# Optimization experiments

Measured on AMD Instinct MI355X. Metric: run time of the kernel, lower is better.

Reference implementation:

```python
import jax, jax.numpy as jnp
import numpy as np

N_NODES = 50000
N_EDGES = 800000
D_IN = 96
D_HID = 96
D_OUT = 96


def _mean_agg(x, src, dst, n_nodes):
    # mean over in-neighbors: agg[v] = mean_{(u->v) in E} x[u]
    msg = x[src]  # [E, d] irregular gather
    summed = jax.ops.segment_sum(msg, dst, num_segments=n_nodes)  # [N, d]
    deg = jax.ops.segment_sum(jnp.ones((src.shape[0],), x.dtype), dst,
                              num_segments=n_nodes)  # [N]
    return summed / jnp.maximum(deg, 1.0)[:, None]


def _sage_conv(x, src, dst, W_self, W_neigh, b):
    agg = _mean_agg(x, src, dst, x.shape[0])
    return x @ W_self + agg @ W_neigh + b


def setup_inputs() -> dict:
    key = jax.random.key(0)
    ks = jax.random.split(key, 9)
    s = 0.05
    return {
        "x": jax.random.normal(ks[0], (N_NODES, D_IN), jnp.float32),
        "src": jax.random.randint(ks[1], (N_EDGES,), 0, N_NODES),
        "dst": jax.random.randint(ks[2], (N_EDGES,), 0, N_NODES),
        "W_self1": jax.random.normal(ks[3], (D_IN, D_HID), jnp.float32) * s,
        "W_neigh1": jax.random.normal(ks[4], (D_IN, D_HID), jnp.float32) * s,
        "b1": jnp.zeros((D_HID,), jnp.float32),
        "W_self2": jax.random.normal(ks[5], (D_HID, D_OUT), jnp.float32) * s,
        "W_neigh2": jax.random.normal(ks[6], (D_HID, D_OUT), jnp.float32) * s,
        "b2": jnp.zeros((D_OUT,), jnp.float32),
    }


def reference(x, src, dst, W_self1, W_neigh1, b1, W_self2, W_neigh2, b2):
    h = _sage_conv(x, src, dst, W_self1, W_neigh1, b1)
    h = jax.nn.relu(h)
    h = _sage_conv(h, src, dst, W_self2, W_neigh2, b2)
    return h
```

## Files before the change

### kernel.cpp

```cpp
#include <hip/hip_runtime.h>
#include <cstdint>
#include <cstddef>

#define NN 50000
#define NE 800000
#define D 96

#define NBUCK 512
#define BSH 7
#define NBU ((NN + 127) >> 7)
#define TILE 8192
#define NTILE ((NE + TILE - 1) / TILE)
#define MAXB 5120

#define AGB 32
#define AGW 1024

typedef __attribute__((ext_vector_type(8))) short bf16x8;
typedef __attribute__((ext_vector_type(4))) float f32x4;


__global__ void bucket_hist(const int* __restrict__ dst, int* __restrict__ bucketCnt) {
    __shared__ int h[NBUCK];
    for (int i = threadIdx.x; i < NBUCK; i += 256) h[i] = 0;
    __syncthreads();
    const int stride = gridDim.x * 256 * 4;
    for (int i = (blockIdx.x * 256 + (int)threadIdx.x) * 4; i < NE; i += stride) {
        int4 d4 = *(const int4*)(dst + i);
        atomicAdd(&h[d4.x >> BSH], 1);
        atomicAdd(&h[d4.y >> BSH], 1);
        atomicAdd(&h[d4.z >> BSH], 1);
        atomicAdd(&h[d4.w >> BSH], 1);
    }
    __syncthreads();
    for (int i = threadIdx.x; i < NBUCK; i += 256)
        if (h[i]) atomicAdd(&bucketCnt[i], h[i]);
}

__global__ void bucket_scan(const int* __restrict__ bucketCnt, int* __restrict__ bucketBase,
                            int* __restrict__ bucketCur) {
    __shared__ int sm[NBUCK];
    const int t = threadIdx.x;
    const int v = bucketCnt[t];
    sm[t] = v;
    __syncthreads();
    for (int s = 1; s < NBUCK; s <<= 1) {
        int u = (t >= s) ? sm[t - s] : 0;
        __syncthreads();
        sm[t] += u;
        __syncthreads();
    }
    const int excl = sm[t] - v;
    bucketBase[t] = excl;
    bucketCur[t] = excl;
}

__launch_bounds__(512)
__global__ void bin_edges(const int* __restrict__ dst, const int* __restrict__ src,
                          int* __restrict__ bucketCur, uint2* __restrict__ pairBuf) {
    __shared__ int hist[NBUCK];
    __shared__ int segStart[NBUCK];
    __shared__ int lcur[NBUCK];
    __shared__ int segBase[NBUCK];
    __shared__ uint2 lpair[TILE];
    const int t = threadIdx.x;
    const int e0 = blockIdx.x * TILE;
    const int cnt = (NE - e0 < TILE) ? (NE - e0) : TILE;

    for (int i = t; i < NBUCK; i += 512) hist[i] = 0;
    __syncthreads();

    for (int i = t * 4; i < cnt; i += 512 * 4) {
        if (i + 3 < cnt) {
            int4 d4 = *(const int4*)(dst + e0 + i);
            atomicAdd(&hist[d4.x >> BSH], 1);
            atomicAdd(&hist[d4.y >> BSH], 1);
            atomicAdd(&hist[d4.z >> BSH], 1);
            atomicAdd(&hist[d4.w >> BSH], 1);
        } else {
            for (int k = i; k < cnt; ++k) atomicAdd(&hist[dst[e0 + k] >> BSH], 1);
        }
    }
    __syncthreads();

    {
        const int v = hist[t];
        segStart[t] = v;
        __syncthreads();
        for (int s = 1; s < NBUCK; s <<= 1) {
            int u = (t >= s) ? segStart[t - s] : 0;
            __syncthreads();
            segStart[t] += u;
            __syncthreads();
        }
        int excl = segStart[t] - v;
        __syncthreads();
        segStart[t] = excl;
        lcur[t] = excl;
    }
    __syncthreads();

    for (int i = t * 4; i < cnt; i += 512 * 4) {
        if (i + 3 < cnt) {
            int4 d4 = *(const int4*)(dst + e0 + i);
            int4 s4 = *(const int4*)(src + e0 + i);
            int p0 = atomicAdd(&lcur[d4.x >> BSH], 1); lpair[p0] = make_uint2(d4.x, s4.x);
            int p1 = atomicAdd(&lcur[d4.y >> BSH], 1); lpair[p1] = make_uint2(d4.y, s4.y);
            int p2 = atomicAdd(&lcur[d4.z >> BSH], 1); lpair[p2] = make_uint2(d4.z, s4.z);
            int p3 = atomicAdd(&lcur[d4.w >> BSH], 1); lpair[p3] = make_uint2(d4.w, s4.w);
        } else {
            for (int k = i; k < cnt; ++k) {
                int d = dst[e0 + k], s = src[e0 + k];
                int p = atomicAdd(&lcur[d >> BSH], 1);
                lpair[p] = make_uint2(d, s);
            }
        }
    }
    __syncthreads();

    {
        int c = hist[t];
        segBase[t] = c ? atomicAdd(&bucketCur[t], c) : 0;
    }
    __syncthreads();

    for (int k = t; k < cnt; k += 512) {
        uint2 p = lpair[k];
        int b = (int)p.x >> BSH;
        pairBuf[(size_t)segBase[b] + (k - segStart[b])] = p;
    }
}

__global__ void csr_build(const uint2* __restrict__ pairBuf, const int* __restrict__ bucketBase,
                          const int* __restrict__ bucketCnt, int* __restrict__ startv,
                          int* __restrict__ csr) {
    __shared__ int h[128], ls[128], cur[128];
    __shared__ int lsrc[MAXB];
    const int b = blockIdx.x;
    const int t = threadIdx.x;
    const int lo = bucketBase[b];
    int cnt = bucketCnt[b];
    if (cnt > MAXB) cnt = MAXB;
    const int node0 = b << BSH;

    if (t < 128) h[t] = 0;
    __syncthreads();
    for (int k = t; k < cnt; k += 256)
        atomicAdd(&h[(int)pairBuf[lo + k].x - node0], 1);
    __syncthreads();
    if (t < 128) ls[t] = h[t];
    __syncthreads();
    for (int s = 1; s < 128; s <<= 1) {
        int u = (t >= s && t < 128) ? ls[t - s] : 0;
        __syncthreads();
        if (t < 128) ls[t] += u;
        __syncthreads();
    }
    if (t < 128) {
        int excl = ls[t] - h[t];
        cur[t] = excl;
        int node = node0 + t;
        if (node < NN) startv[node] = lo + excl;
    }
    __syncthreads();
    for (int k = t; k < cnt; k += 256) {
        uint2 p = pairBuf[lo + k];
        int pos = atomicAdd(&cur[(int)p.x - node0], 1);
        lsrc[pos] = (int)p.y;
    }
    __syncthreads();
    for (int k = t; k < cnt; k += 256) csr[lo + k] = lsrc[k];
}


__device__ inline uint32_t pack2_bf16(float a, float b) {
    uint32_t ua = __float_as_uint(a), ub = __float_as_uint(b);
    ua = (ua + 0x7fffu + ((ua >> 16) & 1u)) >> 16;
    ub = (ub + 0x7fffu + ((ub >> 16) & 1u)) >> 16;
    return ua | (ub << 16);
}

__device__ inline unsigned short pack1_bf16(float a) {
    uint32_t ua = __float_as_uint(a);
    return (unsigned short)((ua + 0x7fffu + ((ua >> 16) & 1u)) >> 16);
}

__device__ inline float bf_lo(uint32_t w) { return __uint_as_float(w << 16); }
__device__ inline float bf_hi(uint32_t w) { return __uint_as_float(w & 0xffff0000u); }


__global__ void repack_both(const float* __restrict__ Ws1, const float* __restrict__ Wn1,
                            const float* __restrict__ Ws2, const float* __restrict__ Wn2,
                            uint32_t* __restrict__ bfg1, uint32_t* __restrict__ bfg2) {
    int t = blockIdx.x * 256 + threadIdx.x;
    if (t >= 4608) return;
    const int layer = (t >= 2304);
    int tt = t - layer * 2304;
    const int isWn = (tt >= 1152);
    const float* __restrict__ W = layer ? (isWn ? Wn2 : Ws2) : (isWn ? Wn1 : Ws1);
    uint32_t* __restrict__ Bfg = layer ? bfg2 : bfg1;
    tt = isWn ? tt - 1152 : tt;
    int s = tt / 384;
    int r = tt - s * 384;
    int nt6 = r >> 6;
    int l = r & 63;
    int col = nt6 * 16 + (l & 15);
    int k0 = 32 * s + 8 * (l >> 4);
    float v[8];
#pragma unroll
    for (int j = 0; j < 8; ++j) v[j] = W[(k0 + j) * D + col];
    uint4 o;
    o.x = pack2_bf16(v[0], v[1]);
    o.y = pack2_bf16(v[2], v[3]);
    o.z = pack2_bf16(v[4], v[5]);
    o.w = pack2_bf16(v[6], v[7]);
    int nt = nt6 + (isWn ? 6 : 0);
    int slot = (s * 12 + nt) * 64 + l;
    *(uint4*)(Bfg + (size_t)slot * 4) = o;
}


__launch_bounds__(256, 2)
__global__ void xform1_mfma(const float* __restrict__ X,
                            const uint32_t* __restrict__ Bfg,
                            const float* __restrict__ Bias,
                            unsigned short* __restrict__ Ys,
                            unsigned short* __restrict__ Yn) {
    __shared__ __align__(16) uint32_t Af[3072];
    const int tid = threadIdx.x;
    const int row0 = blockIdx.x * 64;

#pragma unroll
    for (int it = 0; it < 6; ++it) {
        int flat = (it * 256 + tid) * 4;
        int r = flat / 96, k = flat - (flat / 96) * 96;
        int gr = row0 + r;
        if (gr >= NN) gr = NN - 1;
        float4 xv = *(const float4*)(X + (size_t)gr * D + k);
        int wq = r >> 4, s = k >> 5;
        int lq = ((k >> 3) & 3) * 16 + (r & 15);
        int base = ((wq * 3 + s) * 64 + lq) * 4 + ((k & 7) >> 1);
        Af[base] = pack2_bf16(xv.x, xv.y);
        Af[base + 1] = pack2_bf16(xv.z, xv.w);
    }
    __syncthreads();

    const int w = tid >> 6, l = tid & 63;
    const int cl = l & 15;

    bf16x8 a0 = *(const bf16x8*)&Af[((w * 3 + 0) * 64 + l) * 4];
    bf16x8 a1 = *(const bf16x8*)&Af[((w * 3 + 1) * 64 + l) * 4];
    bf16x8 a2 = *(const bf16x8*)&Af[((w * 3 + 2) * 64 + l) * 4];

    f32x4 acc[12];
#pragma unroll
    for (int nt = 0; nt < 6; ++nt) {
        float bv = Bias[nt * 16 + cl];
        acc[nt] = (f32x4){bv, bv, bv, bv};
    }
#pragma unroll
    for (int nt = 6; nt < 12; ++nt) acc[nt] = (f32x4){0.f, 0.f, 0.f, 0.f};

#pragma unroll
    for (int nt = 0; nt < 12; ++nt) {
        bf16x8 b0 = *(const bf16x8*)(Bfg + ((size_t)((0 * 12 + nt) * 64 + l)) * 4);
        bf16x8 b1 = *(const bf16x8*)(Bfg + ((size_t)((1 * 12 + nt) * 64 + l)) * 4);
        bf16x8 b2 = *(const bf16x8*)(Bfg + ((size_t)((2 * 12 + nt) * 64 + l)) * 4);
        acc[nt] = __builtin_amdgcn_mfma_f32_16x16x32_bf16(a0, b0, acc[nt], 0, 0, 0);
        acc[nt] = __builtin_amdgcn_mfma_f32_16x16x32_bf16(a1, b1, acc[nt], 0, 0, 0);
        acc[nt] = __builtin_amdgcn_mfma_f32_16x16x32_bf16(a2, b2, acc[nt], 0, 0, 0);
    }

    const int grb = row0 + w * 16 + (l >> 4) * 4;
#pragma unroll
    for (int nt = 0; nt < 6; ++nt)
#pragma unroll
        for (int rg = 0; rg < 4; ++rg) {
            int gr = grb + rg;
            if (gr < NN) Ys[(size_t)gr * D + nt * 16 + cl] = pack1_bf16(acc[nt][rg]);
        }
#pragma unroll
    for (int nt = 6; nt < 12; ++nt)
#pragma unroll
        for (int rg = 0; rg < 4; ++rg) {
            int gr = grb + rg;
            if (gr < NN) Yn[(size_t)gr * D + (nt - 6) * 16 + cl] = pack1_bf16(acc[nt][rg]);
        }
}


#define GATHER_BODY(TBL, GET)                                              \
    {                                                                      \
        int e = 0;                                                         \
        for (; e + 7 < dg; e += 8) {                                       \
            _Pragma("unroll")                                              \
            for (int i = 0; i < 8; ++i) {                                  \
                uint32_t wv = TBL[(size_t)(GET(e + i)) * 48 + li];         \
                sx[i] += bf_lo(wv); sy[i] += bf_hi(wv);                    \
            }                                                              \
        }                                                                  \
        if (e + 3 < dg) {                                                  \
            _Pragma("unroll")                                              \
            for (int i = 0; i < 4; ++i) {                                  \
                uint32_t wv = TBL[(size_t)(GET(e + i)) * 48 + li];         \
                sx[i] += bf_lo(wv); sy[i] += bf_hi(wv);                    \
            }                                                              \
            e += 4;                                                        \
        }                                                                  \
        for (; e < dg; ++e) {                                              \
            uint32_t wv = TBL[(size_t)(GET(e)) * 48 + li];                 \
            sx[0] += bf_lo(wv); sy[0] += bf_hi(wv);                        \
        }                                                                  \
    }


__launch_bounds__(256, 4)
__global__ void fused_aggx(const unsigned short* __restrict__ Ys1,
                           const uint32_t* __restrict__ Yn1,
                           const int* __restrict__ csr, const int* __restrict__ startv,
                           const uint32_t* __restrict__ Bfg2, const float* __restrict__ Bias2,
                           unsigned short* __restrict__ Ys2, unsigned short* __restrict__ Yn2) {
    __shared__ __align__(16) uint32_t H[AGB][52];
    __shared__ int lcsr[AGW];
    __shared__ int lsv[AGB + 1];
    const int tid = threadIdx.x;
    const int w = tid >> 6, l = tid & 63;
    const int row0 = blockIdx.x * AGB;
    const int li = (l < 48) ? l : 0;

    if (tid <= AGB) {
        int r = row0 + tid;
        lsv[tid] = (r < NN) ? startv[r] : NE;
    }
    __syncthreads();
    const int e_lo = lsv[0];
    const int wcnt = lsv[AGB] - e_lo;
    const int staged = wcnt < AGW ? wcnt : AGW;
    for (int k = tid; k < staged; k += 256) lcsr[k] = csr[e_lo + k];
    __syncthreads();

    for (int j = 0; j < 8; ++j) {
        const int vl = w * 8 + j;
        const int v = row0 + vl;
        uint32_t hpair = 0;
        if (v < NN) {
            const int sloc = lsv[vl] - e_lo;
            const int dg = lsv[vl + 1] - lsv[vl];
            float sx[8], sy[8];
#pragma unroll
            for (int i = 0; i < 8; ++i) { sx[i] = 0.f; sy[i] = 0.f; }
            if (sloc + dg <= staged) {
#define GET_L(E) lcsr[sloc + (E)]
                GATHER_BODY(Yn1, GET_L)
#undef GET_L
            } else {
                const int* cp = csr + e_lo + sloc;
#define GET_G(E) cp[E]
                GATHER_BODY(Yn1, GET_G)
#undef GET_G
            }
            float ax = ((sx[0] + sx[1]) + (sx[2] + sx[3])) + ((sx[4] + sx[5]) + (sx[6] + sx[7]));
            float ay = ((sy[0] + sy[1]) + (sy[2] + sy[3])) + ((sy[4] + sy[5]) + (sy[6] + sy[7]));
            const float inv = 1.f / (float)(dg > 0 ? dg : 1);
            uint32_t ysp = *(const uint32_t*)(Ys1 + (size_t)v * 96 + 2 * li);
            float r0 = fmaxf(bf_lo(ysp) + ax * inv, 0.f);
            float r1 = fmaxf(bf_hi(ysp) + ay * inv, 0.f);
            hpair = pack2_bf16(r0, r1);
        }
        if (l < 48) H[vl][l] = hpair;
    }
    __syncthreads();

    const int stripe = w >> 1;
    const int hf = w & 1;
    const int cl = l & 15;
    const int kq = l >> 4;

    bf16x8 a0 = *(const bf16x8*)&H[stripe * 16 + cl][0 + 4 * kq];
    bf16x8 a1 = *(const bf16x8*)&H[stripe * 16 + cl][16 + 4 * kq];
    bf16x8 a2 = *(const bf16x8*)&H[stripe * 16 + cl][32 + 4 * kq];

    f32x4 acc[6];
#pragma unroll
    for (int nt = 0; nt < 6; ++nt) {
        float bv = hf ? 0.f : Bias2[nt * 16 + cl];
        acc[nt] = (f32x4){bv, bv, bv, bv};
    }
#pragma unroll
    for (int nt = 0; nt < 6; ++nt) {
        int ntg = hf * 6 + nt;
        bf16x8 b0 = *(const bf16x8*)(Bfg2 + ((size_t)((0 * 12 + ntg) * 64 + l)) * 4);
        bf16x8 b1 = *(const bf16x8*)(Bfg2 + ((size_t)((1 * 12 + ntg) * 64 + l)) * 4);
        bf16x8 b2 = *(const bf16x8*)(Bfg2 + ((size_t)((2 * 12 + ntg) * 64 + l)) * 4);
        acc[nt] = __builtin_amdgcn_mfma_f32_16x16x32_bf16(a0, b0, acc[nt], 0, 0, 0);
        acc[nt] = __builtin_amdgcn_mfma_f32_16x16x32_bf16(a1, b1, acc[nt], 0, 0, 0);
        acc[nt] = __builtin_amdgcn_mfma_f32_16x16x32_bf16(a2, b2, acc[nt], 0, 0, 0);
    }

    const int grb = row0 + stripe * 16 + kq * 4;
    if (hf == 0) {
#pragma unroll
        for (int nt = 0; nt < 6; ++nt)
#pragma unroll
            for (int rg = 0; rg < 4; ++rg) {
                int gr = grb + rg;
                if (gr < NN) Ys2[(size_t)gr * D + nt * 16 + cl] = pack1_bf16(acc[nt][rg]);
            }
    } else {
#pragma unroll
        for (int nt = 0; nt < 6; ++nt)
#pragma unroll
            for (int rg = 0; rg < 4; ++rg) {
                int gr = grb + rg;
                if (gr < NN) Yn2[(size_t)gr * D + nt * 16 + cl] = pack1_bf16(acc[nt][rg]);
            }
    }
}


__launch_bounds__(256, 4)
__global__ void agg_final(const unsigned short* __restrict__ Ys2b,
                          const uint32_t* __restrict__ Yn2,
                          const int* __restrict__ csr, const int* __restrict__ startv,
                          float* __restrict__ out) {
    __shared__ int lcsr[AGW];
    __shared__ int lsv[AGB + 1];
    const int tid = threadIdx.x;
    const int w = tid >> 6, l = tid & 63;
    const int row0 = blockIdx.x * AGB;
    const int li = (l < 48) ? l : 0;

    if (tid <= AGB) {
        int r = row0 + tid;
        lsv[tid] = (r < NN) ? startv[r] : NE;
    }
    __syncthreads();
    const int e_lo = lsv[0];
    const int wcnt = lsv[AGB] - e_lo;
    const int staged = wcnt < AGW ? wcnt : AGW;
    for (int k = tid; k < staged; k += 256) lcsr[k] = csr[e_lo + k];
    __syncthreads();

    for (int j = 0; j < 8; ++j) {
        const int vl = w * 8 + j;
        const int v = row0 + vl;
        if (v >= NN) continue;
        const int sloc = lsv[vl] - e_lo;
        const int dg = lsv[vl + 1] - lsv[vl];
        float sx[8], sy[8];
#pragma unroll
        for (int i = 0; i < 8; ++i) { sx[i] = 0.f; sy[i] = 0.f; }
        if (sloc + dg <= staged) {
#define GET_L(E) lcsr[sloc + (E)]
            GATHER_BODY(Yn2, GET_L)
#undef GET_L
        } else {
            const int* cp = csr + e_lo + sloc;
#define GET_G(E) cp[E]
            GATHER_BODY(Yn2, GET_G)
#undef GET_G
        }
        float ax = ((sx[0] + sx[1]) + (sx[2] + sx[3])) + ((sx[4] + sx[5]) + (sx[6] + sx[7]));
        float ay = ((sy[0] + sy[1]) + (sy[2] + sy[3])) + ((sy[4] + sy[5]) + (sy[6] + sy[7]));
        const float inv = 1.f / (float)(dg > 0 ? dg : 1);
        if (l < 48) {
            const size_t o = (size_t)v * D + 2 * li;
            uint32_t ysp = *(const uint32_t*)(Ys2b + (size_t)v * 96 + 2 * li);
            out[o] = bf_lo(ysp) + ax * inv;
            out[o + 1] = bf_hi(ysp) + ay * inv;
        }
    }
}


extern "C" void kernel_launch(void* const* d_in, const int* in_sizes, int n_in,
                              void* d_out, int out_size, void* d_ws, size_t ws_size,
                              hipStream_t stream) {
    const float* x   = (const float*)d_in[0];
    const int*   src = (const int*)d_in[1];
    const int*   dst = (const int*)d_in[2];
    const float* Ws1 = (const float*)d_in[3];
    const float* Wn1 = (const float*)d_in[4];
    const float* b1  = (const float*)d_in[5];
    const float* Ws2 = (const float*)d_in[6];
    const float* Wn2 = (const float*)d_in[7];
    const float* b2  = (const float*)d_in[8];
    float* out = (float*)d_out;

    char* w = (char*)d_ws;
    int* startv     = (int*)w; w += (size_t)NN * sizeof(int);
    int* bucketCnt  = (int*)w; w += NBUCK * sizeof(int);
    int* bucketBase = (int*)w; w += NBUCK * sizeof(int);
    int* bucketCur  = (int*)w; w += NBUCK * sizeof(int);
    int* csr        = (int*)w; w += (size_t)NE * sizeof(int);
    w = (char*)(((uintptr_t)w + 255) & ~(uintptr_t)255);
    unsigned short* ys1 = (unsigned short*)w; w += (size_t)NN * D * sizeof(unsigned short);
    unsigned short* yn1 = (unsigned short*)w; w += (size_t)NN * D * sizeof(unsigned short);
    unsigned short* ys2 = (unsigned short*)w; w += (size_t)NN * D * sizeof(unsigned short);
    unsigned short* yn2 = (unsigned short*)w; w += (size_t)NN * D * sizeof(unsigned short);
    uint32_t* bfg1 = (uint32_t*)w; w += 36 * 64 * 4 * sizeof(uint32_t);
    uint32_t* bfg2 = (uint32_t*)w; w += 36 * 64 * 4 * sizeof(uint32_t);

    uint2* pairBuf = (uint2*)ys1;

    hipMemsetAsync(bucketCnt, 0, NBUCK * sizeof(int), stream);
    bucket_hist<<<256, 256, 0, stream>>>(dst, bucketCnt);
    bucket_scan<<<1, NBUCK, 0, stream>>>(bucketCnt, bucketBase, bucketCur);
    bin_edges<<<NTILE, 512, 0, stream>>>(dst, src, bucketCur, pairBuf);
    csr_build<<<NBU, 256, 0, stream>>>(pairBuf, bucketBase, bucketCnt, startv, csr);

    repack_both<<<18, 256, 0, stream>>>(Ws1, Wn1, Ws2, Wn2, bfg1, bfg2);

    xform1_mfma<<<(NN + 63) / 64, 256, 0, stream>>>(x, bfg1, b1, ys1, yn1);

    const int agrid = (NN + AGB - 1) / AGB;

    fused_aggx<<<agrid, 256, 0, stream>>>(ys1, (const uint32_t*)yn1, csr, startv,
                                          bfg2, b2, ys2, yn2);

    agg_final<<<agrid, 256, 0, stream>>>(ys2, (const uint32_t*)yn2, csr, startv, out);
}
```

Before: 110.4 us.

## Use fixed-capacity bucket slots, stage stores via LDS, deepen gather loads

```diff
diff --git a/kernel.cpp b/kernel.cpp
--- a/kernel.cpp
+++ b/kernel.cpp
@@ -20,39 +20,8 @@
 typedef __attribute__((ext_vector_type(4))) float f32x4;
 
 
-__global__ void bucket_hist(const int* __restrict__ dst, int* __restrict__ bucketCnt) {
-    __shared__ int h[NBUCK];
-    for (int i = threadIdx.x; i < NBUCK; i += 256) h[i] = 0;
-    __syncthreads();
-    const int stride = gridDim.x * 256 * 4;
-    for (int i = (blockIdx.x * 256 + (int)threadIdx.x) * 4; i < NE; i += stride) {
-        int4 d4 = *(const int4*)(dst + i);
-        atomicAdd(&h[d4.x >> BSH], 1);
-        atomicAdd(&h[d4.y >> BSH], 1);
-        atomicAdd(&h[d4.z >> BSH], 1);
-        atomicAdd(&h[d4.w >> BSH], 1);
-    }
-    __syncthreads();
-    for (int i = threadIdx.x; i < NBUCK; i += 256)
-        if (h[i]) atomicAdd(&bucketCnt[i], h[i]);
-}
-
-__global__ void bucket_scan(const int* __restrict__ bucketCnt, int* __restrict__ bucketBase,
-                            int* __restrict__ bucketCur) {
-    __shared__ int sm[NBUCK];
-    const int t = threadIdx.x;
-    const int v = bucketCnt[t];
-    sm[t] = v;
-    __syncthreads();
-    for (int s = 1; s < NBUCK; s <<= 1) {
-        int u = (t >= s) ? sm[t - s] : 0;
-        __syncthreads();
-        sm[t] += u;
-        __syncthreads();
-    }
-    const int excl = sm[t] - v;
-    bucketBase[t] = excl;
-    bucketCur[t] = excl;
+__global__ void init_cur(int* __restrict__ bucketCur) {
+    bucketCur[threadIdx.x] = (int)threadIdx.x * MAXB;
 }
 
 __launch_bounds__(512)
@@ -131,15 +100,15 @@
     }
 }
 
-__global__ void csr_build(const uint2* __restrict__ pairBuf, const int* __restrict__ bucketBase,
-                          const int* __restrict__ bucketCnt, int* __restrict__ startv,
+__global__ void csr_build(const uint2* __restrict__ pairBuf, const int* __restrict__ bucketCur,
+                          int* __restrict__ deg, int* __restrict__ startv,
                           int* __restrict__ csr) {
     __shared__ int h[128], ls[128], cur[128];
     __shared__ int lsrc[MAXB];
     const int b = blockIdx.x;
     const int t = threadIdx.x;
-    const int lo = bucketBase[b];
-    int cnt = bucketCnt[b];
+    const int lo = b * MAXB;
+    int cnt = bucketCur[b] - lo;
     if (cnt > MAXB) cnt = MAXB;
     const int node0 = b << BSH;
 
@@ -160,7 +129,10 @@
         int excl = ls[t] - h[t];
         cur[t] = excl;
         int node = node0 + t;
-        if (node < NN) startv[node] = lo + excl;
+        if (node < NN) {
+            deg[node] = h[t];
+            startv[node] = lo + excl;
+        }
     }
     __syncthreads();
     for (int k = t; k < cnt; k += 256) {
@@ -226,7 +198,7 @@
                             const float* __restrict__ Bias,
                             unsigned short* __restrict__ Ys,
                             unsigned short* __restrict__ Yn) {
-    __shared__ __align__(16) uint32_t Af[3072];
+    __shared__ __align__(16) uint32_t Af[64 * 52];
     const int tid = threadIdx.x;
     const int row0 = blockIdx.x * 64;
 
@@ -270,40 +242,80 @@
         acc[nt] = __builtin_amdgcn_mfma_f32_16x16x32_bf16(a1, b1, acc[nt], 0, 0, 0);
         acc[nt] = __builtin_amdgcn_mfma_f32_16x16x32_bf16(a2, b2, acc[nt], 0, 0, 0);
     }
-
-    const int grb = row0 + w * 16 + (l >> 4) * 4;
+    __syncthreads();
+
+    unsigned short* Af16 = (unsigned short*)Af;
+    const int lrow = w * 16 + (l >> 4) * 4;
+
 #pragma unroll
     for (int nt = 0; nt < 6; ++nt)
 #pragma unroll
-        for (int rg = 0; rg < 4; ++rg) {
-            int gr = grb + rg;
-            if (gr < NN) Ys[(size_t)gr * D + nt * 16 + cl] = pack1_bf16(acc[nt][rg]);
-        }
+        for (int rg = 0; rg < 4; ++rg)
+            Af16[(lrow + rg) * 104 + nt * 16 + cl] = pack1_bf16(acc[nt][rg]);
+    __syncthreads();
+    {
+        uint32_t* Ysu = (uint32_t*)Ys;
+        const int rowq = tid >> 2, colq = (tid & 3) * 12;
+        if (row0 + rowq < NN) {
+#pragma unroll
+            for (int i = 0; i < 3; ++i)
+                *(uint4*)(Ysu + (size_t)(row0 + rowq) * 48 + colq + i * 4) =
+                    *(const uint4*)&Af[rowq * 52 + colq + i * 4];
+        }
+    }
+    __syncthreads();
+
 #pragma unroll
     for (int nt = 6; nt < 12; ++nt)
 #pragma unroll
-        for (int rg = 0; rg < 4; ++rg) {
-            int gr = grb + rg;
-            if (gr < NN) Yn[(size_t)gr * D + (nt - 6) * 16 + cl] = pack1_bf16(acc[nt][rg]);
-        }
+        for (int rg = 0; rg < 4; ++rg)
+            Af16[(lrow + rg) * 104 + (nt - 6) * 16 + cl] = pack1_bf16(acc[nt][rg]);
+    __syncthreads();
+    {
+        uint32_t* Ynu = (uint32_t*)Yn;
+        const int rowq = tid >> 2, colq = (tid & 3) * 12;
+        if (row0 + rowq < NN) {
+#pragma unroll
+            for (int i = 0; i < 3; ++i)
+                *(uint4*)(Ynu + (size_t)(row0 + rowq) * 48 + colq + i * 4) =
+                    *(const uint4*)&Af[rowq * 52 + colq + i * 4];
+        }
+    }
 }
 
 
 #define GATHER_BODY(TBL, GET)                                              \
     {                                                                      \
         int e = 0;                                                         \
-        for (; e + 7 < dg; e += 8) {                                       \
+        for (; e + 15 < dg; e += 16) {                                     \
+            uint32_t wv[16];                                               \
+            _Pragma("unroll")                                              \
+            for (int i = 0; i < 16; ++i)                                   \
+                wv[i] = TBL[(size_t)(GET(e + i)) * 48 + li];               \
+            _Pragma("unroll")                                              \
+            for (int i = 0; i < 16; ++i) {                                 \
+                sx[i & 3] += bf_lo(wv[i]); sy[i & 3] += bf_hi(wv[i]);      \
+            }                                                              \
+        }                                                                  \
+        if (e + 7 < dg) {                                                  \
+            uint32_t wv[8];                                                \
+            _Pragma("unroll")                                              \
+            for (int i = 0; i < 8; ++i)                                    \
+                wv[i] = TBL[(size_t)(GET(e + i)) * 48 + li];               \
             _Pragma("unroll")                                              \
             for (int i = 0; i < 8; ++i) {                                  \
-                uint32_t wv = TBL[(size_t)(GET(e + i)) * 48 + li];         \
-                sx[i] += bf_lo(wv); sy[i] += bf_hi(wv);                    \
+                sx[i & 3] += bf_lo(wv[i]); sy[i & 3] += bf_hi(wv[i]);      \
             }                                                              \
+            e += 8;                                                        \
         }                                                                  \
         if (e + 3 < dg) {                                                  \
+            uint32_t wv[4];                                                \
+            _Pragma("unroll")                                              \
+            for (int i = 0; i < 4; ++i)                                    \
+                wv[i] = TBL[(size_t)(GET(e + i)) * 48 + li];               \
             _Pragma("unroll")                                              \
             for (int i = 0; i < 4; ++i) {                                  \
-                uint32_t wv = TBL[(size_t)(GET(e + i)) * 48 + li];         \
-                sx[i] += bf_lo(wv); sy[i] += bf_hi(wv);                    \
+                sx[i] += bf_lo(wv[i]); sy[i] += bf_hi(wv[i]);              \
             }                                                              \
             e += 4;                                                        \
         }                                                                  \
@@ -318,11 +330,14 @@
 __global__ void fused_aggx(const unsigned short* __restrict__ Ys1,
                            const uint32_t* __restrict__ Yn1,
                            const int* __restrict__ csr, const int* __restrict__ startv,
+                           const int* __restrict__ deg, const int* __restrict__ bucketCur,
                            const uint32_t* __restrict__ Bfg2, const float* __restrict__ Bias2,
                            unsigned short* __restrict__ Ys2, unsigned short* __restrict__ Yn2) {
-    __shared__ __align__(16) uint32_t H[AGB][52];
+    __shared__ __align__(16) uint32_t H[AGB * 52];
+    __shared__ __align__(16) uint32_t H2[AGB * 52];
     __shared__ int lcsr[AGW];
     __shared__ int lsv[AGB + 1];
+    __shared__ int ldeg[AGB];
     const int tid = threadIdx.x;
     const int w = tid >> 6, l = tid & 63;
     const int row0 = blockIdx.x * AGB;
@@ -330,7 +345,11 @@
 
     if (tid <= AGB) {
         int r = row0 + tid;
-        lsv[tid] = (r < NN) ? startv[r] : NE;
+        lsv[tid] = (r < NN) ? startv[r] : bucketCur[NBU - 1];
+    }
+    if (tid < AGB) {
+        int r = row0 + tid;
+        ldeg[tid] = (r < NN) ? deg[r] : 0;
     }
     __syncthreads();
     const int e_lo = lsv[0];
@@ -345,10 +364,10 @@
         uint32_t hpair = 0;
         if (v < NN) {
             const int sloc = lsv[vl] - e_lo;
-            const int dg = lsv[vl + 1] - lsv[vl];
-            float sx[8], sy[8];
-#pragma unroll
-            for (int i = 0; i < 8; ++i) { sx[i] = 0.f; sy[i] = 0.f; }
+            const int dg = ldeg[vl];
+            float sx[4], sy[4];
+#pragma unroll
+            for (int i = 0; i < 4; ++i) { sx[i] = 0.f; sy[i] = 0.f; }
             if (sloc + dg <= staged) {
 #define GET_L(E) lcsr[sloc + (E)]
                 GATHER_BODY(Yn1, GET_L)
@@ -359,15 +378,15 @@
                 GATHER_BODY(Yn1, GET_G)
 #undef GET_G
             }
-            float ax = ((sx[0] + sx[1]) + (sx[2] + sx[3])) + ((sx[4] + sx[5]) + (sx[6] + sx[7]));
-            float ay = ((sy[0] + sy[1]) + (sy[2] + sy[3])) + ((sy[4] + sy[5]) + (sy[6] + sy[7]));
+            float ax = (sx[0] + sx[1]) + (sx[2] + sx[3]);
+            float ay = (sy[0] + sy[1]) + (sy[2] + sy[3]);
             const float inv = 1.f / (float)(dg > 0 ? dg : 1);
             uint32_t ysp = *(const uint32_t*)(Ys1 + (size_t)v * 96 + 2 * li);
             float r0 = fmaxf(bf_lo(ysp) + ax * inv, 0.f);
             float r1 = fmaxf(bf_hi(ysp) + ay * inv, 0.f);
             hpair = pack2_bf16(r0, r1);
         }
-        if (l < 48) H[vl][l] = hpair;
+        if (l < 48) H[vl * 52 + l] = hpair;
     }
     __syncthreads();
 
@@ -376,9 +395,9 @@
     const int cl = l & 15;
     const int kq = l >> 4;
 
-    bf16x8 a0 = *(const bf16x8*)&H[stripe * 16 + cl][0 + 4 * kq];
-    bf16x8 a1 = *(const bf16x8*)&H[stripe * 16 + cl][16 + 4 * kq];
-    bf16x8 a2 = *(const bf16x8*)&H[stripe * 16 + cl][32 + 4 * kq];
+    bf16x8 a0 = *(const bf16x8*)&H[(stripe * 16 + cl) * 52 + 0 + 4 * kq];
+    bf16x8 a1 = *(const bf16x8*)&H[(stripe * 16 + cl) * 52 + 16 + 4 * kq];
+    bf16x8 a2 = *(const bf16x8*)&H[(stripe * 16 + cl) * 52 + 32 + 4 * kq];
 
     f32x4 acc[6];
 #pragma unroll
@@ -396,24 +415,33 @@
         acc[nt] = __builtin_amdgcn_mfma_f32_16x16x32_bf16(a1, b1, acc[nt], 0, 0, 0);
         acc[nt] = __builtin_amdgcn_mfma_f32_16x16x32_bf16(a2, b2, acc[nt], 0, 0, 0);
     }
-
-    const int grb = row0 + stripe * 16 + kq * 4;
-    if (hf == 0) {
+    __syncthreads();
+
+    {
+        unsigned short* Hb = (unsigned short*)(hf ? H2 : H);
+        const int lrow = stripe * 16 + kq * 4;
 #pragma unroll
         for (int nt = 0; nt < 6; ++nt)
 #pragma unroll
-            for (int rg = 0; rg < 4; ++rg) {
-                int gr = grb + rg;
-                if (gr < NN) Ys2[(size_t)gr * D + nt * 16 + cl] = pack1_bf16(acc[nt][rg]);
-            }
-    } else {
-#pragma unroll
-        for (int nt = 0; nt < 6; ++nt)
-#pragma unroll
-            for (int rg = 0; rg < 4; ++rg) {
-                int gr = grb + rg;
-                if (gr < NN) Yn2[(size_t)gr * D + nt * 16 + cl] = pack1_bf16(acc[nt][rg]);
-            }
+            for (int rg = 0; rg < 4; ++rg)
+                Hb[(lrow + rg) * 104 + nt * 16 + cl] = pack1_bf16(acc[nt][rg]);
+    }
+    __syncthreads();
+
+    {
+        const int row = tid >> 3, colq = (tid & 7) * 6;
+        if (row0 + row < NN) {
+            uint32_t* Ysu = (uint32_t*)Ys2;
+            uint32_t* Ynu = (uint32_t*)Yn2;
+            const size_t gb = (size_t)(row0 + row) * 48 + colq;
+            const int lb = row * 52 + colq;
+#pragma unroll
+            for (int i = 0; i < 3; ++i)
+                *(uint2*)(Ysu + gb + i * 2) = *(const uint2*)&H[lb + i * 2];
+#pragma unroll
+            for (int i = 0; i < 3; ++i)
+                *(uint2*)(Ynu + gb + i * 2) = *(const uint2*)&H2[lb + i * 2];
+        }
     }
 }
 
@@ -422,9 +450,11 @@
 __global__ void agg_final(const unsigned short* __restrict__ Ys2b,
                           const uint32_t* __restrict__ Yn2,
                           const int* __restrict__ csr, const int* __restrict__ startv,
+                          const int* __restrict__ deg, const int* __restrict__ bucketCur,
                           float* __restrict__ out) {
     __shared__ int lcsr[AGW];
     __shared__ int lsv[AGB + 1];
+    __shared__ int ldeg[AGB];
     const int tid = threadIdx.x;
     const int w = tid >> 6, l = tid & 63;
     const int row0 = blockIdx.x * AGB;
@@ -432,7 +462,11 @@
 
     if (tid <= AGB) {
         int r = row0 + tid;
-        lsv[tid] = (r < NN) ? startv[r] : NE;
+        lsv[tid] = (r < NN) ? startv[r] : bucketCur[NBU - 1];
+    }
+    if (tid < AGB) {
+        int r = row0 + tid;
+        ldeg[tid] = (r < NN) ? deg[r] : 0;
     }
     __syncthreads();
     const int e_lo = lsv[0];
@@ -446,10 +480,10 @@
         const int v = row0 + vl;
         if (v >= NN) continue;
         const int sloc = lsv[vl] - e_lo;
-        const int dg = lsv[vl + 1] - lsv[vl];
-        float sx[8], sy[8];
-#pragma unroll
-        for (int i = 0; i < 8; ++i) { sx[i] = 0.f; sy[i] = 0.f; }
+        const int dg = ldeg[vl];
+        float sx[4], sy[4];
+#pragma unroll
+        for (int i = 0; i < 4; ++i) { sx[i] = 0.f; sy[i] = 0.f; }
         if (sloc + dg <= staged) {
 #define GET_L(E) lcsr[sloc + (E)]
             GATHER_BODY(Yn2, GET_L)
@@ -460,8 +494,8 @@
             GATHER_BODY(Yn2, GET_G)
 #undef GET_G
         }
-        float ax = ((sx[0] + sx[1]) + (sx[2] + sx[3])) + ((sx[4] + sx[5]) + (sx[6] + sx[7]));
-        float ay = ((sy[0] + sy[1]) + (sy[2] + sy[3])) + ((sy[4] + sy[5]) + (sy[6] + sy[7]));
+        float ax = (sx[0] + sx[1]) + (sx[2] + sx[3]);
+        float ay = (sy[0] + sy[1]) + (sy[2] + sy[3]);
         const float inv = 1.f / (float)(dg > 0 ? dg : 1);
         if (l < 48) {
             const size_t o = (size_t)v * D + 2 * li;
@@ -488,11 +522,10 @@
     float* out = (float*)d_out;
 
     char* w = (char*)d_ws;
-    int* startv     = (int*)w; w += (size_t)NN * sizeof(int);
-    int* bucketCnt  = (int*)w; w += NBUCK * sizeof(int);
-    int* bucketBase = (int*)w; w += NBUCK * sizeof(int);
-    int* bucketCur  = (int*)w; w += NBUCK * sizeof(int);
-    int* csr        = (int*)w; w += (size_t)NE * sizeof(int);
+    int* startv    = (int*)w; w += (size_t)NN * sizeof(int);
+    int* deg       = (int*)w; w += (size_t)NN * sizeof(int);
+    int* bucketCur = (int*)w; w += NBUCK * sizeof(int);
+    int* csr       = (int*)w; w += (size_t)NBUCK * MAXB * sizeof(int);
     w = (char*)(((uintptr_t)w + 255) & ~(uintptr_t)255);
     unsigned short* ys1 = (unsigned short*)w; w += (size_t)NN * D * sizeof(unsigned short);
     unsigned short* yn1 = (unsigned short*)w; w += (size_t)NN * D * sizeof(unsigned short);
@@ -503,11 +536,9 @@
 
     uint2* pairBuf = (uint2*)ys1;
 
-    hipMemsetAsync(bucketCnt, 0, NBUCK * sizeof(int), stream);
-    bucket_hist<<<256, 256, 0, stream>>>(dst, bucketCnt);
-    bucket_scan<<<1, NBUCK, 0, stream>>>(bucketCnt, bucketBase, bucketCur);
+    init_cur<<<1, NBUCK, 0, stream>>>(bucketCur);
     bin_edges<<<NTILE, 512, 0, stream>>>(dst, src, bucketCur, pairBuf);
-    csr_build<<<NBU, 256, 0, stream>>>(pairBuf, bucketBase, bucketCnt, startv, csr);
+    csr_build<<<NBU, 256, 0, stream>>>(pairBuf, bucketCur, deg, startv, csr);
 
     repack_both<<<18, 256, 0, stream>>>(Ws1, Wn1, Ws2, Wn2, bfg1, bfg2);
 
@@ -515,8 +546,9 @@
 
     const int agrid = (NN + AGB - 1) / AGB;
 
-    fused_aggx<<<agrid, 256, 0, stream>>>(ys1, (const uint32_t*)yn1, csr, startv,
-                                          bfg2, b2, ys2, yn2);
-
-    agg_final<<<agrid, 256, 0, stream>>>(ys2, (const uint32_t*)yn2, csr, startv, out);
-}
+    fused_aggx<<<agrid, 256, 0, stream>>>(ys1, (const uint32_t*)yn1, csr, startv, deg,
+                                          bucketCur, bfg2, b2, ys2, yn2);
+
+    agg_final<<<agrid, 256, 0, stream>>>(ys2, (const uint32_t*)yn2, csr, startv, deg,
+                                         bucketCur, out);
+}
```

New measurement: 114.4 us. +3.6%, slower.
